# Kernel tuning notes

Measured on AMD Instinct MI355X. Metric: run time of the kernel, lower is better.

## Reference

```python
import jax, jax.numpy as jnp
import numpy as np

DIM = 1024
NUM_HEADS = 16
HEAD_DIM = DIM // NUM_HEADS


def _xavier(key, shape):
    fan_out, fan_in = shape[0], shape[1]
    limit = float(np.sqrt(6.0 / (fan_in + fan_out)))
    return jax.random.uniform(key, shape, jnp.float32, -limit, limit)


def setup_inputs() -> dict:
    key = jax.random.key(0)
    k_x, k_in, k_out = jax.random.split(key, 3)
    x = jax.random.normal(k_x, (2, 2048, DIM), jnp.float32)
    in_proj_weight = _xavier(k_in, (3 * DIM, DIM))
    in_proj_bias = jnp.zeros((3 * DIM,), jnp.float32)
    out_proj_weight = _xavier(k_out, (DIM, DIM))
    out_proj_bias = jnp.zeros((DIM,), jnp.float32)
    return {
        "x": x,
        "in_proj_weight": in_proj_weight,
        "in_proj_bias": in_proj_bias,
        "out_proj_weight": out_proj_weight,
        "out_proj_bias": out_proj_bias,
    }


def reference(x, in_proj_weight, in_proj_bias, out_proj_weight, out_proj_bias):
    B, T, C = x.shape
    H, D = NUM_HEADS, HEAD_DIM
    # fused QKV projection: [B,T,3C]
    qkv = x @ in_proj_weight.T + in_proj_bias
    qkv = qkv.reshape(B, T, 3, H, D).transpose(2, 0, 3, 1, 4)  # [3,B,H,T,D]
    q, k, v = qkv[0], qkv[1], qkv[2]
    scale = 1.0 / jnp.sqrt(jnp.asarray(D, x.dtype))
    scores = jnp.einsum("bhqd,bhkd->bhqk", q, k) * scale  # [B,H,T,T]
    attn = jax.nn.softmax(scores, axis=-1)
    out = jnp.einsum("bhqk,bhkd->bhqd", attn, v)  # [B,H,T,D]
    out = out.transpose(0, 2, 1, 3).reshape(B, T, C)
    return out @ out_proj_weight.T + out_proj_bias
```

## Files before the change

### kernel.cpp

```cpp
#include <hip/hip_runtime.h>
#include <stdint.h>

typedef unsigned short bf16u;
typedef unsigned int u32;
typedef __attribute__((ext_vector_type(8))) short s16x8;
typedef __attribute__((ext_vector_type(4))) float f32x4;
typedef __attribute__((ext_vector_type(16))) float f32x16;

#define QSCALE 0.18033688011112042f

static __device__ __forceinline__ bf16u f2bf(float f) {
    uint32_t u = __float_as_uint(f);
    uint32_t r = (u + 0x7FFFu + ((u >> 16) & 1u)) >> 16;
    return (bf16u)r;
}
static __device__ __forceinline__ u32 pack2(float lo, float hi) {
    return (u32)f2bf(lo) | ((u32)f2bf(hi) << 16);
}
static __device__ __forceinline__ u32 cvtpk(float lo, float hi) {
    u32 r;
    asm("v_cvt_pk_bf16_f32 %0, %1, %2" : "=v"(r) : "v"(lo), "v"(hi));
    return r;
}

static __device__ __forceinline__ f32x4 mfma16(s16x8 a, s16x8 b, f32x4 c) {
    return __builtin_amdgcn_mfma_f32_16x16x32_bf16(a, b, c, 0, 0, 0);
}
static __device__ __forceinline__ f32x16 mfma32(s16x8 a, s16x8 b, f32x16 c) {
    return __builtin_amdgcn_mfma_f32_32x32x16_bf16(a, b, c, 0, 0, 0);
}

#define GLDS(gsrc, ldst)                                                        \
    __builtin_amdgcn_global_load_lds(                                           \
        (const __attribute__((address_space(1))) void*)(gsrc),                  \
        (__attribute__((address_space(3))) void*)(ldst), 16, 0, 0)

__global__ __launch_bounds__(256) void cvt_f32_bf16_kernel(
    const float* __restrict__ in, bf16u* __restrict__ out, int n) {
    union Pack { bf16u h[8]; uint4 u; };
    for (int i = (blockIdx.x * 256 + threadIdx.x) * 8; i < n; i += gridDim.x * 256 * 8) {
        const float4 a = *(const float4*)(in + i);
        const float4 b = *(const float4*)(in + i + 4);
        Pack p;
        p.h[0] = f2bf(a.x); p.h[1] = f2bf(a.y); p.h[2] = f2bf(a.z); p.h[3] = f2bf(a.w);
        p.h[4] = f2bf(b.x); p.h[5] = f2bf(b.y); p.h[6] = f2bf(b.z); p.h[7] = f2bf(b.w);
        *(uint4*)(out + i) = p.u;
    }
}

template <int MODE>
__global__ __launch_bounds__(256) void gemm_bt_kernel(
    const bf16u* __restrict__ A, const bf16u* __restrict__ Bt,
    const float* __restrict__ bias, float* __restrict__ Cf,
    bf16u* __restrict__ Qo, bf16u* __restrict__ Ko, bf16u* __restrict__ Vto,
    int M, int N, int K) {
    __shared__ bf16u As[128 * 32];
    __shared__ bf16u Bs[128 * 32];
    const int tid  = threadIdx.x;
    const int wave = tid >> 6, lane = tid & 63;
    const int wr = wave >> 1, wc = wave & 1;
    const int ri = lane & 15, hi = lane >> 4;
    const int m0 = blockIdx.x * 128, n0 = blockIdx.y * 128;

    f32x4 acc[4][4];
#pragma unroll
    for (int i = 0; i < 4; ++i)
#pragma unroll
        for (int j = 0; j < 4; ++j) acc[i][j] = (f32x4){0.f, 0.f, 0.f, 0.f};

    for (int k0 = 0; k0 < K; k0 += 32) {
        __syncthreads();
#pragma unroll
        for (int it = 0; it < 2; ++it) {
            const int chunk = it * 4 + wave;
            const int e = chunk * 512 + lane * 8;
            const int r = e >> 5, c = e & 31;
            GLDS(A  + (size_t)(m0 + r) * K + (k0 + c), As + chunk * 512);
            GLDS(Bt + (size_t)(n0 + r) * K + (k0 + c), Bs + chunk * 512);
        }
        __syncthreads();
        s16x8 af[4], bfr[4];
#pragma unroll
        for (int i = 0; i < 4; ++i) {
            af[i]  = *(const s16x8*)(As + (wr * 64 + i * 16 + ri) * 32 + hi * 8);
            bfr[i] = *(const s16x8*)(Bs + (wc * 64 + i * 16 + ri) * 32 + hi * 8);
        }
#pragma unroll
        for (int i = 0; i < 4; ++i)
#pragma unroll
            for (int j = 0; j < 4; ++j) acc[i][j] = mfma16(af[i], bfr[j], acc[i][j]);
    }

#pragma unroll
    for (int i = 0; i < 4; ++i) {
#pragma unroll
        for (int j = 0; j < 4; ++j) {
#pragma unroll
            for (int r = 0; r < 4; ++r) {
                const int row = m0 + wr * 64 + i * 16 + hi * 4 + r;
                const int col = n0 + wc * 64 + j * 16 + ri;
                const float v = acc[i][j][r] + bias[col];
                if constexpr (MODE == 0) {
                    Cf[(size_t)row * N + col] = v;
                } else {
                    const int which = col >> 10, h = (col >> 6) & 15, d = col & 63;
                    const int b = row >> 11, t = row & 2047;
                    const int bh = b * 16 + h;
                    if (which == 2) {
                        Vto[(((size_t)bh) * 64 + d) * 2048 + t] = f2bf(v);
                    } else if (which == 0) {
                        Qo[(((size_t)bh) * 2048 + t) * 64 + d] = f2bf(v * QSCALE);
                    } else {
                        Ko[(((size_t)bh) * 2048 + t) * 64 + d] = f2bf(v);
                    }
                }
            }
        }
    }
}

__global__ __launch_bounds__(512) void attn_kernel(
    const bf16u* __restrict__ Q, const bf16u* __restrict__ K,
    const bf16u* __restrict__ Vt, bf16u* __restrict__ O) {
    __shared__ uint4 smem4[4 * 64 * 72 * 2 / 16];
    bf16u* Ks0 = (bf16u*)smem4;
    bf16u* Vs0 = Ks0 + 64 * 72;
    bf16u* Ks1 = Vs0 + 64 * 72;
    bf16u* Vs1 = Ks1 + 64 * 72;
    float* mrg = (float*)smem4;

    const int tid = threadIdx.x, lane = tid & 63;
    const int wave = tid >> 6, wg = wave & 3, half = wave >> 2;
    const int ri = lane & 31, hi = lane >> 5;
    const int bh = blockIdx.y, b = bh >> 4, h = bh & 15;
    const int q0 = blockIdx.x * 128 + wg * 32;
    const bf16u* Qb = Q  + (size_t)bh * 2048 * 64;
    const bf16u* Kb = K  + (size_t)bh * 2048 * 64;
    const bf16u* Vb = Vt + (size_t)bh * 64 * 2048;

    s16x8 qf[4];
#pragma unroll
    for (int c = 0; c < 4; ++c)
        qf[c] = *(const s16x8*)(Qb + (size_t)(q0 + ri) * 64 + c * 16 + hi * 8);

    const bf16u* Ksh = half ? Ks1 : Ks0;
    const bf16u* Vsh = half ? Vs1 : Vs0;

    f32x16 oacc[2];
#pragma unroll
    for (int r = 0; r < 16; ++r) { oacc[0][r] = 0.f; oacc[1][r] = 0.f; }
    float m = -1e30f, lsum = 0.f;

    const int srow = tid >> 3, sc = tid & 7;
    for (int kt = 0; kt < 16; ++kt) {
        const uint4 k0 = *(const uint4*)(Kb + (size_t)(kt * 64 + srow) * 64 + sc * 8);
        const uint4 k1 = *(const uint4*)(Kb + (size_t)((kt + 16) * 64 + srow) * 64 + sc * 8);
        const uint4 v0 = *(const uint4*)(Vb + (size_t)srow * 2048 + kt * 64 + sc * 8);
        const uint4 v1 = *(const uint4*)(Vb + (size_t)srow * 2048 + (kt + 16) * 64 + sc * 8);
        __syncthreads();
        *(uint4*)(Ks0 + srow * 72 + sc * 8) = k0;
        *(uint4*)(Ks1 + srow * 72 + sc * 8) = k1;
        *(uint4*)(Vs0 + srow * 72 + sc * 8) = v0;
        *(uint4*)(Vs1 + srow * 72 + sc * 8) = v1;
        __syncthreads();

        f32x16 sa[2];
#pragma unroll
        for (int r = 0; r < 16; ++r) { sa[0][r] = 0.f; sa[1][r] = 0.f; }
#pragma unroll
        for (int kb2 = 0; kb2 < 2; ++kb2) {
            const int row = kb2 * 32 + ri;
#pragma unroll
            for (int c = 0; c < 4; ++c) {
                s16x8 kf = *(const s16x8*)(Ksh + row * 72 + (2 * c + hi) * 8);
                sa[kb2] = mfma32(kf, qf[c], sa[kb2]);
            }
        }

        float pmt[16];
#pragma unroll
        for (int r = 0; r < 16; ++r) pmt[r] = fmaxf(sa[0][r], sa[1][r]);
#pragma unroll
        for (int s = 8; s > 0; s >>= 1)
#pragma unroll
            for (int r = 0; r < s; ++r) pmt[r] = fmaxf(pmt[r], pmt[r + s]);
        const float pm = fmaxf(pmt[0], __shfl_xor(pmt[0], 32));

        if (!__all(pm <= m + 8.f)) {
            const float mn = fmaxf(m, pm);
            const float al = __builtin_amdgcn_exp2f(m - mn);
            m = mn;
            lsum *= al;
#pragma unroll
            for (int r = 0; r < 16; ++r) { oacc[0][r] *= al; oacc[1][r] *= al; }
        }

        float rs0 = 0.f, rs1 = 0.f, rs2 = 0.f, rs3 = 0.f;
#pragma unroll
        for (int kb2 = 0; kb2 < 2; ++kb2)
#pragma unroll
            for (int r = 0; r < 16; ++r) {
                const float p = __builtin_amdgcn_exp2f(sa[kb2][r] - m);
                sa[kb2][r] = p;
                if ((r & 3) == 0) rs0 += p;
                else if ((r & 3) == 1) rs1 += p;
                else if ((r & 3) == 2) rs2 += p;
                else rs3 += p;
            }
        float rs = (rs0 + rs1) + (rs2 + rs3);
        rs += __shfl_xor(rs, 32);
        lsum += rs;

        s16x8 pb[4];
#pragma unroll
        for (int blk = 0; blk < 2; ++blk) {
            u32 pk[4][2];
#pragma unroll
            for (int j = 0; j < 4; ++j) {
                pk[j][0] = cvtpk(sa[blk][4 * j + 0], sa[blk][4 * j + 1]);
                pk[j][1] = cvtpk(sa[blk][4 * j + 2], sa[blk][4 * j + 3]);
            }
#pragma unroll
            for (int halfq = 0; halfq < 2; ++halfq) {
                const int ja = 2 * halfq, jb = ja + 1;
                u32 keep0 = hi ? pk[jb][0] : pk[ja][0];
                u32 keep1 = hi ? pk[jb][1] : pk[ja][1];
                u32 send0 = hi ? pk[ja][0] : pk[jb][0];
                u32 send1 = hi ? pk[ja][1] : pk[jb][1];
                u32 recv0 = __shfl_xor(send0, 32);
                u32 recv1 = __shfl_xor(send1, 32);
                union { u32 w[4]; s16x8 v; } pu;
                pu.w[0] = hi ? recv0 : keep0;
                pu.w[1] = hi ? recv1 : keep1;
                pu.w[2] = hi ? keep0 : recv0;
                pu.w[3] = hi ? keep1 : recv1;
                pb[blk * 2 + halfq] = pu.v;
            }
        }

#pragma unroll
        for (int dt = 0; dt < 2; ++dt) {
            const int row = dt * 32 + ri;
#pragma unroll
            for (int k4 = 0; k4 < 4; ++k4) {
                s16x8 vf = *(const s16x8*)(Vsh + row * 72 + (2 * k4 + hi) * 8);
                oacc[dt] = mfma32(vf, pb[k4], oacc[dt]);
            }
        }
    }

    __syncthreads();
    if (half) {
        float* p = mrg + (wg * 64 + lane) * 35;
        p[0] = m; p[1] = lsum;
#pragma unroll
        for (int r = 0; r < 16; ++r) { p[2 + r] = oacc[0][r]; p[18 + r] = oacc[1][r]; }
    }
    __syncthreads();
    if (!half) {
        const float* p = mrg + (wg * 64 + lane) * 35;
        const float m1 = p[0], l1 = p[1];
        const float mn = fmaxf(m, m1);
        const float a0 = __builtin_amdgcn_exp2f(m - mn);
        const float a1 = __builtin_amdgcn_exp2f(m1 - mn);
        const float inv = 1.f / (lsum * a0 + l1 * a1);
        const int t = q0 + ri;
        bf16u* Ob = O + ((size_t)b * 2048 + t) * 1024 + h * 64;
#pragma unroll
        for (int dt = 0; dt < 2; ++dt)
#pragma unroll
            for (int j = 0; j < 4; ++j) {
                const int d0 = dt * 32 + j * 8 + hi * 4;
                const float e0 = (oacc[dt][4 * j + 0] * a0 + p[2 + dt * 16 + 4 * j + 0] * a1) * inv;
                const float e1 = (oacc[dt][4 * j + 1] * a0 + p[2 + dt * 16 + 4 * j + 1] * a1) * inv;
                const float e2 = (oacc[dt][4 * j + 2] * a0 + p[2 + dt * 16 + 4 * j + 2] * a1) * inv;
                const float e3 = (oacc[dt][4 * j + 3] * a0 + p[2 + dt * 16 + 4 * j + 3] * a1) * inv;
                uint2 wv; wv.x = pack2(e0, e1); wv.y = pack2(e2, e3);
                *(uint2*)(Ob + d0) = wv;
            }
    }
}

extern "C" void kernel_launch(void* const* d_in, const int* in_sizes, int n_in,
                              void* d_out, int out_size, void* d_ws, size_t ws_size,
                              hipStream_t stream) {
    const float* x     = (const float*)d_in[0];
    const float* w_in  = (const float*)d_in[1];
    const float* b_in  = (const float*)d_in[2];
    const float* w_out = (const float*)d_in[3];
    const float* b_out = (const float*)d_in[4];
    float* out = (float*)d_out;

    char* ws = (char*)d_ws;
    bf16u* xb    = (bf16u*)(ws);
    bf16u* wqkvb = (bf16u*)(ws + 8388608);
    bf16u* woutb = (bf16u*)(ws + 14680064);
    bf16u* qb    = (bf16u*)(ws + 16777216);
    bf16u* kb    = (bf16u*)(ws + 25165824);
    bf16u* vtb   = (bf16u*)(ws + 33554432);
    bf16u* attnb = xb;

    cvt_f32_bf16_kernel<<<2048, 256, 0, stream>>>(x, xb, 4096 * 1024);
    cvt_f32_bf16_kernel<<<1536, 256, 0, stream>>>(w_in, wqkvb, 3072 * 1024);
    cvt_f32_bf16_kernel<<<512, 256, 0, stream>>>(w_out, woutb, 1024 * 1024);

    gemm_bt_kernel<1><<<dim3(32, 24), 256, 0, stream>>>(
        xb, wqkvb, b_in, nullptr, qb, kb, vtb, 4096, 3072, 1024);

    attn_kernel<<<dim3(16, 32), 512, 0, stream>>>(qb, kb, vtb, attnb);

    gemm_bt_kernel<0><<<dim3(32, 8), 256, 0, stream>>>(
        attnb, woutb, b_out, out, nullptr, nullptr, nullptr, 4096, 1024, 1024);
}
```

Baseline: 151.2 us.

## Double-buffer K/V shared tiles and prefetch next tile during compute

Result: slower. 155.1 us (+2.6%).

```diff
diff --git a/kernel.cpp b/kernel.cpp
--- a/kernel.cpp
+++ b/kernel.cpp
@@ -122,15 +122,20 @@
 __global__ __launch_bounds__(512) void attn_kernel(
     const bf16u* __restrict__ Q, const bf16u* __restrict__ K,
     const bf16u* __restrict__ Vt, bf16u* __restrict__ O) {
-    __shared__ uint4 smem4[4 * 64 * 72 * 2 / 16];
-    bf16u* Ks0 = (bf16u*)smem4;
-    bf16u* Vs0 = Ks0 + 64 * 72;
-    bf16u* Ks1 = Vs0 + 64 * 72;
-    bf16u* Vs1 = Ks1 + 64 * 72;
+    __shared__ uint4 smem4[8 * 64 * 72 * 2 / 16];
+    bf16u* base = (bf16u*)smem4;
+    bf16u* KsA0 = base;
+    bf16u* VsA0 = base + 4608;
+    bf16u* KsA1 = base + 9216;
+    bf16u* VsA1 = base + 13824;
+    bf16u* KsB0 = base + 18432;
+    bf16u* VsB0 = base + 23040;
+    bf16u* KsB1 = base + 27648;
+    bf16u* VsB1 = base + 32256;
     float* mrg = (float*)smem4;
 
     const int tid = threadIdx.x, lane = tid & 63;
-    const int wave = tid >> 6, wg = wave & 3, half = wave >> 2;
+    const int wave = tid >> 6, wg = wave & 3, kvh = wave >> 2;
     const int ri = lane & 31, hi = lane >> 5;
     const int bh = blockIdx.y, b = bh >> 4, h = bh & 15;
     const int q0 = blockIdx.x * 128 + wg * 32;
@@ -143,121 +148,142 @@
     for (int c = 0; c < 4; ++c)
         qf[c] = *(const s16x8*)(Qb + (size_t)(q0 + ri) * 64 + c * 16 + hi * 8);
 
-    const bf16u* Ksh = half ? Ks1 : Ks0;
-    const bf16u* Vsh = half ? Vs1 : Vs0;
-
     f32x16 oacc[2];
 #pragma unroll
     for (int r = 0; r < 16; ++r) { oacc[0][r] = 0.f; oacc[1][r] = 0.f; }
     float m = -1e30f, lsum = 0.f;
 
     const int srow = tid >> 3, sc = tid & 7;
-    for (int kt = 0; kt < 16; ++kt) {
-        const uint4 k0 = *(const uint4*)(Kb + (size_t)(kt * 64 + srow) * 64 + sc * 8);
-        const uint4 k1 = *(const uint4*)(Kb + (size_t)((kt + 16) * 64 + srow) * 64 + sc * 8);
-        const uint4 v0 = *(const uint4*)(Vb + (size_t)srow * 2048 + kt * 64 + sc * 8);
-        const uint4 v1 = *(const uint4*)(Vb + (size_t)srow * 2048 + (kt + 16) * 64 + sc * 8);
+
+    {
+        const uint4 k0 = *(const uint4*)(Kb + (size_t)(0 * 64 + srow) * 64 + sc * 8);
+        const uint4 k1 = *(const uint4*)(Kb + (size_t)(16 * 64 + srow) * 64 + sc * 8);
+        const uint4 v0 = *(const uint4*)(Vb + (size_t)srow * 2048 + 0 * 64 + sc * 8);
+        const uint4 v1 = *(const uint4*)(Vb + (size_t)srow * 2048 + 16 * 64 + sc * 8);
+        *(uint4*)(KsA0 + srow * 72 + sc * 8) = k0;
+        *(uint4*)(KsA1 + srow * 72 + sc * 8) = k1;
+        *(uint4*)(VsA0 + srow * 72 + sc * 8) = v0;
+        *(uint4*)(VsA1 + srow * 72 + sc * 8) = v1;
         __syncthreads();
-        *(uint4*)(Ks0 + srow * 72 + sc * 8) = k0;
-        *(uint4*)(Ks1 + srow * 72 + sc * 8) = k1;
-        *(uint4*)(Vs0 + srow * 72 + sc * 8) = v0;
-        *(uint4*)(Vs1 + srow * 72 + sc * 8) = v1;
-        __syncthreads();
-
-        f32x16 sa[2];
-#pragma unroll
-        for (int r = 0; r < 16; ++r) { sa[0][r] = 0.f; sa[1][r] = 0.f; }
-#pragma unroll
-        for (int kb2 = 0; kb2 < 2; ++kb2) {
-            const int row = kb2 * 32 + ri;
-#pragma unroll
-            for (int c = 0; c < 4; ++c) {
-                s16x8 kf = *(const s16x8*)(Ksh + row * 72 + (2 * c + hi) * 8);
-                sa[kb2] = mfma32(kf, qf[c], sa[kb2]);
-            }
-        }
-
-        float pmt[16];
-#pragma unroll
-        for (int r = 0; r < 16; ++r) pmt[r] = fmaxf(sa[0][r], sa[1][r]);
-#pragma unroll
-        for (int s = 8; s > 0; s >>= 1)
-#pragma unroll
-            for (int r = 0; r < s; ++r) pmt[r] = fmaxf(pmt[r], pmt[r + s]);
-        const float pm = fmaxf(pmt[0], __shfl_xor(pmt[0], 32));
-
-        if (!__all(pm <= m + 8.f)) {
-            const float mn = fmaxf(m, pm);
-            const float al = __builtin_amdgcn_exp2f(m - mn);
-            m = mn;
-            lsum *= al;
-#pragma unroll
-            for (int r = 0; r < 16; ++r) { oacc[0][r] *= al; oacc[1][r] *= al; }
-        }
-
-        float rs0 = 0.f, rs1 = 0.f, rs2 = 0.f, rs3 = 0.f;
-#pragma unroll
-        for (int kb2 = 0; kb2 < 2; ++kb2)
-#pragma unroll
-            for (int r = 0; r < 16; ++r) {
-                const float p = __builtin_amdgcn_exp2f(sa[kb2][r] - m);
-                sa[kb2][r] = p;
-                if ((r & 3) == 0) rs0 += p;
-                else if ((r & 3) == 1) rs1 += p;
-                else if ((r & 3) == 2) rs2 += p;
-                else rs3 += p;
-            }
-        float rs = (rs0 + rs1) + (rs2 + rs3);
-        rs += __shfl_xor(rs, 32);
-        lsum += rs;
-
-        s16x8 pb[4];
-#pragma unroll
-        for (int blk = 0; blk < 2; ++blk) {
-            u32 pk[4][2];
-#pragma unroll
-            for (int j = 0; j < 4; ++j) {
-                pk[j][0] = cvtpk(sa[blk][4 * j + 0], sa[blk][4 * j + 1]);
-                pk[j][1] = cvtpk(sa[blk][4 * j + 2], sa[blk][4 * j + 3]);
-            }
-#pragma unroll
-            for (int halfq = 0; halfq < 2; ++halfq) {
-                const int ja = 2 * halfq, jb = ja + 1;
-                u32 keep0 = hi ? pk[jb][0] : pk[ja][0];
-                u32 keep1 = hi ? pk[jb][1] : pk[ja][1];
-                u32 send0 = hi ? pk[ja][0] : pk[jb][0];
-                u32 send1 = hi ? pk[ja][1] : pk[jb][1];
-                u32 recv0 = __shfl_xor(send0, 32);
-                u32 recv1 = __shfl_xor(send1, 32);
-                union { u32 w[4]; s16x8 v; } pu;
-                pu.w[0] = hi ? recv0 : keep0;
-                pu.w[1] = hi ? recv1 : keep1;
-                pu.w[2] = hi ? keep0 : recv0;
-                pu.w[3] = hi ? keep1 : recv1;
-                pb[blk * 2 + halfq] = pu.v;
-            }
-        }
-
-#pragma unroll
-        for (int dt = 0; dt < 2; ++dt) {
-            const int row = dt * 32 + ri;
-#pragma unroll
-            for (int k4 = 0; k4 < 4; ++k4) {
-                s16x8 vf = *(const s16x8*)(Vsh + row * 72 + (2 * k4 + hi) * 8);
-                oacc[dt] = mfma32(vf, pb[k4], oacc[dt]);
-            }
-        }
-    }
-
-    __syncthreads();
-    if (half) {
+    }
+
+#define TILE_BODY(ktv, KC0, VC0, KC1, VC1, KN0, VN0, KN1, VN1)                    \
+    {                                                                             \
+        const int ktn = (ktv) + 1;                                                \
+        uint4 k0n, k1n, v0n, v1n;                                                 \
+        if (ktn < 16) {                                                           \
+            k0n = *(const uint4*)(Kb + (size_t)(ktn * 64 + srow) * 64 + sc * 8);  \
+            k1n = *(const uint4*)(Kb + (size_t)((ktn + 16) * 64 + srow) * 64 + sc * 8); \
+            v0n = *(const uint4*)(Vb + (size_t)srow * 2048 + ktn * 64 + sc * 8);  \
+            v1n = *(const uint4*)(Vb + (size_t)srow * 2048 + (ktn + 16) * 64 + sc * 8); \
+        }                                                                         \
+        const bf16u* Ksh = kvh ? (KC1) : (KC0);                                   \
+        const bf16u* Vsh = kvh ? (VC1) : (VC0);                                   \
+        f32x16 sa[2];                                                             \
+        _Pragma("unroll")                                                         \
+        for (int r = 0; r < 16; ++r) { sa[0][r] = 0.f; sa[1][r] = 0.f; }          \
+        __builtin_amdgcn_s_setprio(1);                                            \
+        _Pragma("unroll")                                                         \
+        for (int kb2 = 0; kb2 < 2; ++kb2) {                                       \
+            const int row = kb2 * 32 + ri;                                        \
+            _Pragma("unroll")                                                     \
+            for (int c = 0; c < 4; ++c) {                                         \
+                s16x8 kf = *(const s16x8*)(Ksh + row * 72 + (2 * c + hi) * 8);    \
+                sa[kb2] = mfma32(kf, qf[c], sa[kb2]);                             \
+            }                                                                     \
+        }                                                                         \
+        __builtin_amdgcn_s_setprio(0);                                            \
+        float pmt[16];                                                            \
+        _Pragma("unroll")                                                         \
+        for (int r = 0; r < 16; ++r) pmt[r] = fmaxf(sa[0][r], sa[1][r]);          \
+        _Pragma("unroll")                                                         \
+        for (int s = 8; s > 0; s >>= 1)                                           \
+            _Pragma("unroll")                                                     \
+            for (int r = 0; r < s; ++r) pmt[r] = fmaxf(pmt[r], pmt[r + s]);       \
+        const float pm = fmaxf(pmt[0], __shfl_xor(pmt[0], 32));                   \
+        if (!__all(pm <= m + 8.f)) {                                              \
+            const float mn = fmaxf(m, pm);                                        \
+            const float al = __builtin_amdgcn_exp2f(m - mn);                      \
+            m = mn;                                                               \
+            lsum *= al;                                                           \
+            _Pragma("unroll")                                                     \
+            for (int r = 0; r < 16; ++r) { oacc[0][r] *= al; oacc[1][r] *= al; }  \
+        }                                                                         \
+        float rs0 = 0.f, rs1 = 0.f, rs2 = 0.f, rs3 = 0.f;                         \
+        _Pragma("unroll")                                                         \
+        for (int kb2 = 0; kb2 < 2; ++kb2)                                         \
+            _Pragma("unroll")                                                     \
+            for (int r = 0; r < 16; ++r) {                                        \
+                const float p = __builtin_amdgcn_exp2f(sa[kb2][r] - m);           \
+                sa[kb2][r] = p;                                                   \
+                if ((r & 3) == 0) rs0 += p;                                       \
+                else if ((r & 3) == 1) rs1 += p;                                  \
+                else if ((r & 3) == 2) rs2 += p;                                  \
+                else rs3 += p;                                                    \
+            }                                                                     \
+        float rs = (rs0 + rs1) + (rs2 + rs3);                                     \
+        rs += __shfl_xor(rs, 32);                                                 \
+        lsum += rs;                                                               \
+        s16x8 pb[4];                                                              \
+        _Pragma("unroll")                                                         \
+        for (int blk = 0; blk < 2; ++blk) {                                       \
+            u32 pk[4][2];                                                         \
+            _Pragma("unroll")                                                     \
+            for (int j = 0; j < 4; ++j) {                                         \
+                pk[j][0] = cvtpk(sa[blk][4 * j + 0], sa[blk][4 * j + 1]);         \
+                pk[j][1] = cvtpk(sa[blk][4 * j + 2], sa[blk][4 * j + 3]);         \
+            }                                                                     \
+            _Pragma("unroll")                                                     \
+            for (int halfq = 0; halfq < 2; ++halfq) {                             \
+                const int ja = 2 * halfq, jb = ja + 1;                            \
+                u32 keep0 = hi ? pk[jb][0] : pk[ja][0];                           \
+                u32 keep1 = hi ? pk[jb][1] : pk[ja][1];                           \
+                u32 send0 = hi ? pk[ja][0] : pk[jb][0];                           \
+                u32 send1 = hi ? pk[ja][1] : pk[jb][1];                           \
+                u32 recv0 = __shfl_xor(send0, 32);                                \
+                u32 recv1 = __shfl_xor(send1, 32);                                \
+                union { u32 w[4]; s16x8 v; } pu;                                  \
+                pu.w[0] = hi ? recv0 : keep0;                                     \
+                pu.w[1] = hi ? recv1 : keep1;                                     \
+                pu.w[2] = hi ? keep0 : recv0;                                     \
+                pu.w[3] = hi ? keep1 : recv1;                                     \
+                pb[blk * 2 + halfq] = pu.v;                                       \
+            }                                                                     \
+        }                                                                         \
+        __builtin_amdgcn_s_setprio(1);                                            \
+        _Pragma("unroll")                                                         \
+        for (int dt = 0; dt < 2; ++dt) {                                          \
+            const int row = dt * 32 + ri;                                         \
+            _Pragma("unroll")                                                     \
+            for (int k4 = 0; k4 < 4; ++k4) {                                      \
+                s16x8 vf = *(const s16x8*)(Vsh + row * 72 + (2 * k4 + hi) * 8);   \
+                oacc[dt] = mfma32(vf, pb[k4], oacc[dt]);                          \
+            }                                                                     \
+        }                                                                         \
+        __builtin_amdgcn_s_setprio(0);                                            \
+        if (ktn < 16) {                                                           \
+            *(uint4*)((KN0) + srow * 72 + sc * 8) = k0n;                          \
+            *(uint4*)((KN1) + srow * 72 + sc * 8) = k1n;                          \
+            *(uint4*)((VN0) + srow * 72 + sc * 8) = v0n;                          \
+            *(uint4*)((VN1) + srow * 72 + sc * 8) = v1n;                          \
+        }                                                                         \
+        __syncthreads();                                                          \
+    }
+
+    for (int kt2 = 0; kt2 < 8; ++kt2) {
+        TILE_BODY(kt2 * 2,     KsA0, VsA0, KsA1, VsA1, KsB0, VsB0, KsB1, VsB1);
+        TILE_BODY(kt2 * 2 + 1, KsB0, VsB0, KsB1, VsB1, KsA0, VsA0, KsA1, VsA1);
+    }
+#undef TILE_BODY
+
+    if (kvh) {
         float* p = mrg + (wg * 64 + lane) * 35;
         p[0] = m; p[1] = lsum;
 #pragma unroll
         for (int r = 0; r < 16; ++r) { p[2 + r] = oacc[0][r]; p[18 + r] = oacc[1][r]; }
     }
     __syncthreads();
-    if (!half) {
+    if (!kvh) {
         const float* p = mrg + (wg * 64 + lane) * 35;
         const float m1 = p[0], l1 = p[1];
         const float mn = fmaxf(m, m1);
```

## Halve attention block to 256 threads with 64 queries per block

Applied to the files above, without the earlier changes.

Measured after the change: 258.9 us. +71.2%, slower.

```diff
diff --git a/kernel.cpp b/kernel.cpp
--- a/kernel.cpp
+++ b/kernel.cpp
@@ -119,7 +119,7 @@
     }
 }
 
-__global__ __launch_bounds__(512) void attn_kernel(
+__global__ __launch_bounds__(256, 4) void attn_kernel(
     const bf16u* __restrict__ Q, const bf16u* __restrict__ K,
     const bf16u* __restrict__ Vt, bf16u* __restrict__ O) {
     __shared__ uint4 smem4[4 * 64 * 72 * 2 / 16];
@@ -130,10 +130,10 @@
     float* mrg = (float*)smem4;
 
     const int tid = threadIdx.x, lane = tid & 63;
-    const int wave = tid >> 6, wg = wave & 3, half = wave >> 2;
+    const int wave = tid >> 6, wg = wave & 1, kvh = wave >> 1;
     const int ri = lane & 31, hi = lane >> 5;
     const int bh = blockIdx.y, b = bh >> 4, h = bh & 15;
-    const int q0 = blockIdx.x * 128 + wg * 32;
+    const int q0 = blockIdx.x * 64 + wg * 32;
     const bf16u* Qb = Q  + (size_t)bh * 2048 * 64;
     const bf16u* Kb = K  + (size_t)bh * 2048 * 64;
     const bf16u* Vb = Vt + (size_t)bh * 64 * 2048;
@@ -143,25 +143,35 @@
     for (int c = 0; c < 4; ++c)
         qf[c] = *(const s16x8*)(Qb + (size_t)(q0 + ri) * 64 + c * 16 + hi * 8);
 
-    const bf16u* Ksh = half ? Ks1 : Ks0;
-    const bf16u* Vsh = half ? Vs1 : Vs0;
+    const bf16u* Ksh = kvh ? Ks1 : Ks0;
+    const bf16u* Vsh = kvh ? Vs1 : Vs0;
 
     f32x16 oacc[2];
 #pragma unroll
     for (int r = 0; r < 16; ++r) { oacc[0][r] = 0.f; oacc[1][r] = 0.f; }
     float m = -1e30f, lsum = 0.f;
 
-    const int srow = tid >> 3, sc = tid & 7;
     for (int kt = 0; kt < 16; ++kt) {
-        const uint4 k0 = *(const uint4*)(Kb + (size_t)(kt * 64 + srow) * 64 + sc * 8);
-        const uint4 k1 = *(const uint4*)(Kb + (size_t)((kt + 16) * 64 + srow) * 64 + sc * 8);
-        const uint4 v0 = *(const uint4*)(Vb + (size_t)srow * 2048 + kt * 64 + sc * 8);
-        const uint4 v1 = *(const uint4*)(Vb + (size_t)srow * 2048 + (kt + 16) * 64 + sc * 8);
+        uint4 k0[2], k1[2], v0[2], v1[2];
+#pragma unroll
+        for (int p = 0; p < 2; ++p) {
+            const int chunkid = p * 256 + tid;
+            const int row = chunkid >> 3, c = chunkid & 7;
+            k0[p] = *(const uint4*)(Kb + (size_t)(kt * 64 + row) * 64 + c * 8);
+            k1[p] = *(const uint4*)(Kb + (size_t)((kt + 16) * 64 + row) * 64 + c * 8);
+            v0[p] = *(const uint4*)(Vb + (size_t)row * 2048 + kt * 64 + c * 8);
+            v1[p] = *(const uint4*)(Vb + (size_t)row * 2048 + (kt + 16) * 64 + c * 8);
+        }
         __syncthreads();
-        *(uint4*)(Ks0 + srow * 72 + sc * 8) = k0;
-        *(uint4*)(Ks1 + srow * 72 + sc * 8) = k1;
-        *(uint4*)(Vs0 + srow * 72 + sc * 8) = v0;
-        *(uint4*)(Vs1 + srow * 72 + sc * 8) = v1;
+#pragma unroll
+        for (int p = 0; p < 2; ++p) {
+            const int chunkid = p * 256 + tid;
+            const int row = chunkid >> 3, c = chunkid & 7;
+            *(uint4*)(Ks0 + row * 72 + c * 8) = k0[p];
+            *(uint4*)(Ks1 + row * 72 + c * 8) = k1[p];
+            *(uint4*)(Vs0 + row * 72 + c * 8) = v0[p];
+            *(uint4*)(Vs1 + row * 72 + c * 8) = v1[p];
+        }
         __syncthreads();
 
         f32x16 sa[2];
@@ -250,14 +260,14 @@
     }
 
     __syncthreads();
-    if (half) {
+    if (kvh) {
         float* p = mrg + (wg * 64 + lane) * 35;
         p[0] = m; p[1] = lsum;
 #pragma unroll
         for (int r = 0; r < 16; ++r) { p[2 + r] = oacc[0][r]; p[18 + r] = oacc[1][r]; }
     }
     __syncthreads();
-    if (!half) {
+    if (!kvh) {
         const float* p = mrg + (wg * 64 + lane) * 35;
         const float m1 = p[0], l1 = p[1];
         const float mn = fmaxf(m, m1);
@@ -307,7 +317,7 @@
     gemm_bt_kernel<1><<<dim3(32, 24), 256, 0, stream>>>(
         xb, wqkvb, b_in, nullptr, qb, kb, vtb, 4096, 3072, 1024);
 
-    attn_kernel<<<dim3(16, 32), 512, 0, stream>>>(qb, kb, vtb, attnb);
+    attn_kernel<<<dim3(32, 32), 256, 0, stream>>>(qb, kb, vtb, attnb);
 
     gemm_bt_kernel<0><<<dim3(32, 8), 256, 0, stream>>>(
         attnb, woutb, b_out, out, nullptr, nullptr, nullptr, 4096, 1024, 1024);
```
